# Optimization experiments

Measured on AMD Instinct MI355X. Metric: run time of the kernel, lower is better.

## Reference

```python
import jax, jax.numpy as jnp
import numpy as np

HIDDEN = 1024
NUM_HEADS = 16
HEAD_DIM = HIDDEN // NUM_HEADS
WINDOW = 512


def setup_inputs() -> dict:
    key = jax.random.key(0)
    ks = jax.random.split(key, 6)
    b, s = 2, 4096
    x = jax.random.normal(ks[0], (b, s, HIDDEN), dtype=jnp.float32)
    attention_mask = jnp.ones((b, s), dtype=jnp.int32)
    scale = 1.0 / np.sqrt(HIDDEN)
    Wq = jax.random.normal(ks[1], (HIDDEN, HIDDEN), dtype=jnp.float32) * scale
    Wk = jax.random.normal(ks[2], (HIDDEN, HIDDEN), dtype=jnp.float32) * scale
    Wv = jax.random.normal(ks[3], (HIDDEN, HIDDEN), dtype=jnp.float32) * scale
    Wo = jax.random.normal(ks[4], (HIDDEN, HIDDEN), dtype=jnp.float32) * scale
    return {"x": x, "attention_mask": attention_mask,
            "Wq": Wq, "Wk": Wk, "Wv": Wv, "Wo": Wo}


def reference(x, attention_mask, Wq, Wk, Wv, Wo):
    b, s, d = x.shape
    # nn.Linear computes x @ W.T
    q = (x @ Wq.T).reshape(b, s, NUM_HEADS, HEAD_DIM).transpose(0, 2, 1, 3)
    k = (x @ Wk.T).reshape(b, s, NUM_HEADS, HEAD_DIM).transpose(0, 2, 1, 3)
    v = (x @ Wv.T).reshape(b, s, NUM_HEADS, HEAD_DIM).transpose(0, 2, 1, 3)
    # [b,h,s,s] scores
    scores = jnp.einsum('bhqd,bhkd->bhqk', q, k) / np.sqrt(HEAD_DIM)
    # causal sliding-window mask: allow j <= i and j >= i - window + 1
    i = jnp.arange(s)[:, None]
    j = jnp.arange(s)[None, :]
    window_mask = (j <= i) & (j >= i - WINDOW + 1)  # [s,s]
    neg_inf = jnp.finfo(scores.dtype).min
    scores = jnp.where(window_mask[None, None], scores, neg_inf)
    pad = attention_mask.astype(bool)[:, None, None, :]  # [b,1,1,s]
    scores = jnp.where(pad, scores, neg_inf)
    probs = jax.nn.softmax(scores, axis=-1)
    out = jnp.einsum('bhqk,bhkd->bhqd', probs, v)
    out = out.transpose(0, 2, 1, 3).reshape(b, s, d)
    return out @ Wo.T
```

## Files before the change

### kernel.cpp

```cpp
#include <hip/hip_runtime.h>
#include <cstdint>
#include <cstddef>

#define HID 1024
#define SEQ 4096
#define NB  2
#define NH  16
#define HD  64
#define WIN 512
#define TOK (NB*SEQ)

typedef _Float16 f16x8 __attribute__((ext_vector_type(8)));
typedef _Float16 f16x4 __attribute__((ext_vector_type(4)));
typedef float    f32x4 __attribute__((ext_vector_type(4)));

__global__ __launch_bounds__(256)
void convert_kernel(const float* __restrict__ X, const float* __restrict__ w0,
                    const float* __restrict__ w1, const float* __restrict__ w2,
                    const float* __restrict__ w3,
                    _Float16* __restrict__ Xh, _Float16* __restrict__ Wh) {
  const int bi = blockIdx.x;
  const float* src; _Float16* dst; size_t off;
  if (bi < 4096) {
    src = X; dst = Xh; off = (size_t)bi * 2048;
  } else {
    const int wi = bi - 4096, z = wi >> 9;
    src = (z == 0) ? w0 : (z == 1) ? w1 : (z == 2) ? w2 : w3;
    dst = Wh + (size_t)z * HID * HID;
    off = (size_t)(wi & 511) * 2048;
  }
  const size_t i = off + (size_t)threadIdx.x * 8;
  f32x4 a = *(const f32x4*)(src + i);
  f32x4 b = *(const f32x4*)(src + i + 4);
  f16x8 o;
#pragma unroll
  for (int r = 0; r < 4; ++r) { o[r] = (_Float16)a[r]; o[r+4] = (_Float16)b[r]; }
  *(f16x8*)(dst + i) = o;
}

__device__ __forceinline__ void gload16(const void* g, void* lds) {
  __builtin_amdgcn_global_load_lds(
      (__attribute__((address_space(1))) void*)(void*)g,
      (__attribute__((address_space(3))) void*)lds, 16, 0, 0);
}

#define VMW_(n) asm volatile("s_waitcnt vmcnt(" #n ")" ::: "memory")
#define VMW(n) VMW_(n)

#define STG(GP, RP) {                                                         \
    gload16((GP) + (size_t)srow*HID + scol,     (RP) + ldo0);                 \
    gload16((GP) + (size_t)(srow+8)*HID + scol, (RP) + ldo1);                 \
  }

#define RDA(DST, HP) {                                                        \
    _Pragma("unroll")                                                         \
    for (int mm = 0; mm < 4; ++mm) {                                          \
      const int ar = (wr*16 + mm*32 + l15) * 64;                              \
      DST[mm][0] = *(const f16x8*)((HP) + ar + ((quad ^ swl) << 3));          \
      DST[mm][1] = *(const f16x8*)((HP) + ar + (((4 + quad) ^ swl) << 3));    \
    } }

#define RDB(DST, HP) {                                                        \
    _Pragma("unroll")                                                         \
    for (int nn = 0; nn < 2; ++nn) {                                          \
      const int br = (nn*64 + wc*16 + l15) * 64;                              \
      DST[nn][0] = *(const f16x8*)((HP) + br + ((quad ^ swl) << 3));          \
      DST[nn][1] = *(const f16x8*)((HP) + br + (((4 + quad) ^ swl) << 3));    \
    } }

#define CORE(QM, QN, AF, BV, VMN) {                                           \
    __builtin_amdgcn_s_barrier();                                             \
    __builtin_amdgcn_s_setprio(1);                                            \
    _Pragma("unroll")                                                         \
    for (int mm = 0; mm < 4; ++mm)                                            \
      _Pragma("unroll")                                                       \
      for (int nn = 0; nn < 2; ++nn) {                                        \
        acc[QM*4+mm][QN*2+nn] = __builtin_amdgcn_mfma_f32_16x16x32_f16(       \
            AF[mm][0], BV[nn][0], acc[QM*4+mm][QN*2+nn], 0, 0, 0);            \
        acc[QM*4+mm][QN*2+nn] = __builtin_amdgcn_mfma_f32_16x16x32_f16(       \
            AF[mm][1], BV[nn][1], acc[QM*4+mm][QN*2+nn], 0, 0, 0);            \
      }                                                                       \
    __builtin_amdgcn_s_setprio(0);                                            \
    VMW(VMN);                                                                 \
    __builtin_amdgcn_s_barrier();                                             \
    asm volatile("" ::: "memory");                                            \
  }

__global__ __launch_bounds__(512, 2)
void gemm_qkv8p_kernel(const _Float16* __restrict__ X,
                       const _Float16* __restrict__ Wh,
                       _Float16* __restrict__ Q,
                       _Float16* __restrict__ Kb,
                       _Float16* __restrict__ Vt) {
  __shared__ __align__(16) _Float16 sAb[2][2][128*64];
  __shared__ __align__(16) _Float16 sBb[2][2][128*64];

  const int bid = blockIdx.x;
  const int xcd = bid & 7, idx = bid >> 3;
  const int mt = xcd*4 + (idx & 3);
  const int nt = idx >> 2;
  const int M0  = mt * 256;
  const int N0g = nt * 256;
  const int z   = N0g >> 10;
  const int N0c = N0g & 1023;

  const _Float16* Arow = X  + (size_t)M0 * HID;
  const _Float16* Brow = Wh + (size_t)z * HID * HID + (size_t)N0c * HID;

  const int tid  = threadIdx.x;
  const int lane = tid & 63, wave = tid >> 6;
  const int wr = wave >> 2, wc = wave & 3;
  const int l15 = lane & 15, quad = lane >> 4;
  const int swl = l15 & 7;

  const int srow = wave*16 + (lane >> 3);
  const int scol = ((lane & 7) ^ (lane >> 3)) << 3;
  const int ldo0 = (wave*128 + lane) * 8;
  const int ldo1 = ldo0 + 64*8;

  f32x4 acc[8][4] = {};
  f16x8 af0[4][2], af1[4][2], bv0[2][2], bv1[2][2];

  STG(Brow,               sBb[0][0]);
  STG(Arow,               sAb[0][0]);
  STG(Arow + 128*HID,     sAb[0][1]);
  STG(Brow + 128*HID,     sBb[0][1]);
  STG(Brow + 64,          sBb[1][0]);
  STG(Arow + 64,          sAb[1][0]);
  VMW(8);
  __builtin_amdgcn_s_barrier();
  asm volatile("" ::: "memory");

  RDB(bv0, sBb[0][0]);

#pragma unroll 1
  for (int t = 0; t < 14; t += 2) {
    const int k1 = (t+1)*64, k2 = (t+2)*64, k3 = (t+3)*64;
    RDA(af0, sAb[0][0]);  STG(Arow + 128*HID + k1, sAb[1][1]);  CORE(0,0,af0,bv0,8);
    RDA(af1, sAb[0][1]);  STG(Brow + 128*HID + k1, sBb[1][1]);  CORE(1,0,af1,bv0,8);
    RDB(bv1, sBb[0][1]);  STG(Brow + k2,           sBb[0][0]);  CORE(1,1,af1,bv1,8);
    RDB(bv0, sBb[1][0]);  STG(Arow + k2,           sAb[0][0]);  CORE(0,1,af0,bv1,8);
    RDA(af0, sAb[1][0]);  STG(Arow + 128*HID + k2, sAb[0][1]);  CORE(0,0,af0,bv0,8);
    RDA(af1, sAb[1][1]);  STG(Brow + 128*HID + k2, sBb[0][1]);  CORE(1,0,af1,bv0,8);
    RDB(bv1, sBb[1][1]);  STG(Brow + k3,           sBb[1][0]);  CORE(1,1,af1,bv1,8);
    RDB(bv0, sBb[0][0]);  STG(Arow + k3,           sAb[1][0]);  CORE(0,1,af0,bv1,8);
  }
  {
    const int k1 = 15*64;
    RDA(af0, sAb[0][0]);  STG(Arow + 128*HID + k1, sAb[1][1]);  CORE(0,0,af0,bv0,8);
    RDA(af1, sAb[0][1]);  STG(Brow + 128*HID + k1, sBb[1][1]);  CORE(1,0,af1,bv0,8);
    RDB(bv1, sBb[0][1]);                                        CORE(1,1,af1,bv1,6);
    RDB(bv0, sBb[1][0]);                                        CORE(0,1,af0,bv1,4);
  }
  {
    RDA(af0, sAb[1][0]);                                        CORE(0,0,af0,bv0,2);
    RDA(af1, sAb[1][1]);                                        CORE(1,0,af1,bv0,0);
    RDB(bv1, sBb[1][1]);                                        CORE(1,1,af1,bv1,0);
                                                                CORE(0,1,af0,bv1,0);
  }

  if (z < 2) {
    _Float16* C = (z == 0) ? Q : Kb;
    const float scl = (z == 0) ? 0.18033688011f : 1.0f;
#pragma unroll
    for (int mf = 0; mf < 8; ++mf) {
      const int row = M0 + (mf >> 2)*128 + wr*16 + (mf & 3)*32 + quad*4;
#pragma unroll
      for (int nf = 0; nf < 4; ++nf) {
        const int col = N0c + (nf >> 1)*128 + (nf & 1)*64 + wc*16 + l15;
#pragma unroll
        for (int r = 0; r < 4; ++r)
          C[(size_t)(row + r)*HID + col] = (_Float16)(acc[mf][nf][r] * scl);
      }
    }
  } else {
#pragma unroll
    for (int mf = 0; mf < 8; ++mf) {
      const int row = M0 + (mf >> 2)*128 + wr*16 + (mf & 3)*32 + quad*4;
#pragma unroll
      for (int nf = 0; nf < 4; ++nf) {
        const int col = N0c + (nf >> 1)*128 + (nf & 1)*64 + wc*16 + l15;
        f16x4 v;
#pragma unroll
        for (int r = 0; r < 4; ++r) v[r] = (_Float16)acc[mf][nf][r];
        *(f16x4*)(Vt + (size_t)col*TOK + row) = v;
      }
    }
  }
}

__device__ __forceinline__ void gemm_mainloop(
    const _Float16* __restrict__ A, const _Float16* __restrict__ W,
    _Float16* sA, _Float16* sB, f32x4 (&acc)[4][4], int m0, int n0) {
  const int tid  = threadIdx.x;
  const int lane = tid & 63;
  const int wave = tid >> 6;
  const int wm = wave >> 1, wn = wave & 1;
  const int l15 = lane & 15, quad = lane >> 4;

  const int o0 = tid * 16;
  const int o1 = o0 + 4096;
  const _Float16* a0 = A + (size_t)(m0 + (o0 >> 6)) * HID + ((o0 & 63) >> 1);
  const _Float16* a1 = A + (size_t)(m0 + (o1 >> 6)) * HID + ((o1 & 63) >> 1);
  const _Float16* w0 = W + (size_t)(n0 + (o0 >> 6)) * HID + ((o0 & 63) >> 1);
  const _Float16* w1 = W + (size_t)(n0 + (o1 >> 6)) * HID + ((o1 & 63) >> 1);
  _Float16* la0 = sA + (o0 >> 1);
  _Float16* la1 = sA + (o1 >> 1);
  _Float16* lb0 = sB + (o0 >> 1);
  _Float16* lb1 = sB + (o1 >> 1);

  const int aoff = (wm*64 + l15)*32 + quad*8;
  const int boff = (wn*64 + l15)*32 + quad*8;

  for (int k0 = 0; k0 < HID; k0 += 64) {
    __syncthreads();
    gload16(a0 + k0,      la0);
    gload16(a1 + k0,      la1);
    gload16(a0 + k0 + 32, la0 + 4096);
    gload16(a1 + k0 + 32, la1 + 4096);
    gload16(w0 + k0,      lb0);
    gload16(w1 + k0,      lb1);
    gload16(w0 + k0 + 32, lb0 + 4096);
    gload16(w1 + k0 + 32, lb1 + 4096);
    __syncthreads();
#pragma unroll
    for (int s = 0; s < 2; ++s) {
      const int sb = s * 4096;
      f16x8 af[4], wf[4];
#pragma unroll
      for (int t = 0; t < 4; ++t) {
        af[t] = *(const f16x8*)(sA + sb + aoff + t*512);
        wf[t] = *(const f16x8*)(sB + sb + boff + t*512);
      }
#pragma unroll
      for (int i = 0; i < 4; ++i)
#pragma unroll
        for (int j = 0; j < 4; ++j)
          acc[i][j] = __builtin_amdgcn_mfma_f32_16x16x32_f16(af[i], wf[j], acc[i][j], 0, 0, 0);
    }
  }
}

__global__ __launch_bounds__(256, 3)
void gemm_o_kernel(const _Float16* __restrict__ A,
                   const _Float16* __restrict__ Wo,
                   float* __restrict__ C) {
  __shared__ __align__(16) _Float16 sA[128*64];
  __shared__ __align__(16) _Float16 sB[128*64];
  const int i  = blockIdx.x;
  const int g  = i & 7;
  const int j  = i >> 3;
  const int mi = j & 7;
  const int n0 = (j >> 3) * 128;
  const int m0 = (g*8 + mi) * 128;
  f32x4 acc[4][4] = {};
  gemm_mainloop(A, Wo, sA, sB, acc, m0, n0);

  const int tid  = threadIdx.x;
  const int lane = tid & 63;
  const int wave = tid >> 6;
  const int wm = wave >> 1, wn = wave & 1;
  const int l15 = lane & 15, quad = lane >> 4;
#pragma unroll
  for (int tm = 0; tm < 4; ++tm)
#pragma unroll
    for (int tn = 0; tn < 4; ++tn) {
      const int row = m0 + wm*64 + tm*16 + quad*4;
      const int col = n0 + wn*64 + tn*16 + l15;
#pragma unroll
      for (int r = 0; r < 4; ++r)
        C[(size_t)(row + r)*HID + col] = acc[tm][tn][r];
    }
}

__global__ __launch_bounds__(512, 4)
void attn_kernel(const _Float16* __restrict__ Q, const _Float16* __restrict__ Kb,
                 const _Float16* __restrict__ Vt, const int* __restrict__ AM,
                 _Float16* __restrict__ O) {
  __shared__ __align__(16) _Float16 sK[128*64];
  __shared__ __align__(16) _Float16 sV[64*128];
  __shared__ __align__(16) _Float16 sP[8*32*64];
  __shared__ int sOK;

  const int bi = blockIdx.x;
  const int g  = bi & 7;
  const int jj = bi >> 3;
  const int combo = g*4 + (jj >> 4);
  const int h = combo & 15, b = combo >> 4;
  const int qb = jj & 15;

  const int tid  = threadIdx.x;
  const int lane = tid & 63, wave = tid >> 6;
  const int l15 = lane & 15, quad = lane >> 4;

  const int q0 = qb * 256;
  const int qw = q0 + wave * 32;

  const int swz = l15 & 7;
  const int cA8 = ((quad ^ swz) << 3);
  const int cB8 = (((quad + 4) ^ swz) << 3);

  f16x8 qf[2][2];
#pragma unroll
  for (int ns = 0; ns < 2; ++ns) {
    const size_t qbse = (size_t)(b*SEQ + qw + ns*16 + l15)*HID + h*HD + quad*8;
    qf[ns][0] = *(const f16x8*)(Q + qbse);
    qf[ns][1] = *(const f16x8*)(Q + qbse + 32);
  }

  int stage_lo = (q0 - (WIN - 1));
  stage_lo = (stage_lo < 0) ? 0 : (stage_lo & ~127);
  const int nst = (q0 + 256 - stage_lo) >> 7;

  if (tid == 0) sOK = 1;
  __syncthreads();
  {
    int ok = 1;
    for (int j = stage_lo + tid; j < q0 + 256; j += 512) ok &= (AM[b*SEQ + j] != 0);
    if (!ok) sOK = 0;
  }
  __syncthreads();
  const bool allok = (sOK != 0);

  const int prow = tid >> 3;
  const int pc   = tid & 7;
  const int pco  = ((pc ^ (prow & 7)) << 3);
  f16x8 pk0, pk1, pv0, pv1;
  {
    const _Float16* kp = Kb + (size_t)(b*SEQ + stage_lo + prow)*HID + h*HD + pco;
    pk0 = *(const f16x8*)kp;
    pk1 = *(const f16x8*)(kp + (size_t)64*HID);
    const _Float16* vp = Vt + (size_t)(h*HD + prow)*TOK + b*SEQ + stage_lo + pco;
    pv0 = *(const f16x8*)vp;
    pv1 = *(const f16x8*)(vp + 64);
  }

  float l_run[2] = {0.0f, 0.0f};
  f32x4 o[4][2] = {};
  _Float16* myP = sP + wave * (32*64);

  for (int st = 0; st < nst; ++st) {
    const int j0st = stage_lo + st*128;
    __syncthreads();
    *(f16x8*)(sK + prow*64 + pc*8)        = pk0;
    *(f16x8*)(sK + (64 + prow)*64 + pc*8) = pk1;
    *(f16x8*)(sV + prow*128 + pc*8)       = pv0;
    *(f16x8*)(sV + prow*128 + 64 + pc*8)  = pv1;
    __syncthreads();
    if (st + 1 < nst) {
      const int jn = j0st + 128;
      const _Float16* kp = Kb + (size_t)(b*SEQ + jn + prow)*HID + h*HD + pco;
      pk0 = *(const f16x8*)kp;
      pk1 = *(const f16x8*)(kp + (size_t)64*HID);
      const _Float16* vp = Vt + (size_t)(h*HD + prow)*TOK + b*SEQ + jn + pco;
      pv0 = *(const f16x8*)vp;
      pv1 = *(const f16x8*)(vp + 64);
    }

#pragma unroll
    for (int s = 0; s < 2; ++s) {
      const int j0 = j0st + s*64;
      if (j0 > qw + 31 || j0 + 63 < qw - (WIN - 1)) continue;
      const bool interior = (j0 + 63 <= qw) && (j0 >= qw - (WIN - 32));

      f32x4 sc[4][2] = {};
#pragma unroll
      for (int t = 0; t < 4; ++t) {
        const f16x8 kf0 = *(const f16x8*)(sK + (s*64 + t*16 + l15)*64 + cA8);
        const f16x8 kf1 = *(const f16x8*)(sK + (s*64 + t*16 + l15)*64 + cB8);
        sc[t][0] = __builtin_amdgcn_mfma_f32_16x16x32_f16(kf0, qf[0][0], sc[t][0], 0, 0, 0);
        sc[t][0] = __builtin_amdgcn_mfma_f32_16x16x32_f16(kf1, qf[0][1], sc[t][0], 0, 0, 0);
        sc[t][1] = __builtin_amdgcn_mfma_f32_16x16x32_f16(kf0, qf[1][0], sc[t][1], 0, 0, 0);
        sc[t][1] = __builtin_amdgcn_mfma_f32_16x16x32_f16(kf1, qf[1][1], sc[t][1], 0, 0, 0);
      }

      if (!allok) {
#pragma unroll
        for (int t = 0; t < 4; ++t)
#pragma unroll
          for (int r = 0; r < 4; ++r) {
            const float ad = (AM[b*SEQ + j0 + t*16 + quad*4 + r] == 0) ? -2e30f : 0.0f;
            sc[t][0][r] += ad;
            sc[t][1][r] += ad;
          }
      }

#pragma unroll
      for (int ns = 0; ns < 2; ++ns) {
        if (!interior) {
          const int i = qw + ns*16 + l15;
#pragma unroll
          for (int t = 0; t < 4; ++t)
#pragma unroll
            for (int r = 0; r < 4; ++r) {
              const int j = j0 + t*16 + quad*4 + r;
              const bool valid = (unsigned)(i - j) < WIN;
              sc[t][ns][r] = valid ? sc[t][ns][r] : -1e30f;
            }
        }
        float sum = 0.0f;
#pragma unroll
        for (int t = 0; t < 4; ++t) {
          f16x4 pvv;
#pragma unroll
          for (int r = 0; r < 4; ++r) {
            const float p = __builtin_amdgcn_exp2f(sc[t][ns][r]);
            sum += p;
            pvv[r] = (_Float16)p;
          }
          const int paddr = (ns*16 + l15)*64 + (((2*t + (quad >> 1)) ^ swz) << 3) + (quad & 1)*4;
          *(f16x4*)(myP + paddr) = pvv;
        }
        sum += __shfl_xor(sum, 16, 64);
        sum += __shfl_xor(sum, 32, 64);
        l_run[ns] += sum;
      }

      const f16x8 pf00 = *(const f16x8*)(myP + l15*64 + cA8);
      const f16x8 pf01 = *(const f16x8*)(myP + l15*64 + cB8);
      const f16x8 pf10 = *(const f16x8*)(myP + (16 + l15)*64 + cA8);
      const f16x8 pf11 = *(const f16x8*)(myP + (16 + l15)*64 + cB8);
#pragma unroll
      for (int dt = 0; dt < 4; ++dt) {
        const f16x8 vf0 = *(const f16x8*)(sV + (dt*16 + l15)*128 + s*64 + cA8);
        const f16x8 vf1 = *(const f16x8*)(sV + (dt*16 + l15)*128 + s*64 + cB8);
        o[dt][0] = __builtin_amdgcn_mfma_f32_16x16x32_f16(vf0, pf00, o[dt][0], 0, 0, 0);
        o[dt][0] = __builtin_amdgcn_mfma_f32_16x16x32_f16(vf1, pf01, o[dt][0], 0, 0, 0);
        o[dt][1] = __builtin_amdgcn_mfma_f32_16x16x32_f16(vf0, pf10, o[dt][1], 0, 0, 0);
        o[dt][1] = __builtin_amdgcn_mfma_f32_16x16x32_f16(vf1, pf11, o[dt][1], 0, 0, 0);
      }
    }
  }

  const float inv[2] = {1.0f / fmaxf(l_run[0], 1e-30f), 1.0f / fmaxf(l_run[1], 1e-30f)};
#pragma unroll
  for (int ns = 0; ns < 2; ++ns) {
    const size_t ob = (size_t)(b*SEQ + qw + ns*16 + l15)*HID + h*HD + quad*4;
#pragma unroll
    for (int dt = 0; dt < 4; ++dt) {
      f16x4 v;
#pragma unroll
      for (int r = 0; r < 4; ++r) v[r] = (_Float16)(o[dt][ns][r] * inv[ns]);
      *(f16x4*)(O + ob + dt*16) = v;
    }
  }
}

extern "C" void kernel_launch(void* const* d_in, const int* in_sizes, int n_in,
                              void* d_out, int out_size, void* d_ws, size_t ws_size,
                              hipStream_t stream) {
  const float* X  = (const float*)d_in[0];
  const int*   AM = (const int*)d_in[1];
  const float* Wq = (const float*)d_in[2];
  const float* Wk = (const float*)d_in[3];
  const float* Wv = (const float*)d_in[4];
  const float* Wo = (const float*)d_in[5];
  float* out = (float*)d_out;

  _Float16* Xh = (_Float16*)d_ws;
  _Float16* Wh = Xh + (size_t)TOK*HID;
  _Float16* Qb = Wh + (size_t)4*HID*HID;
  _Float16* Kb = Qb + (size_t)TOK*HID;
  _Float16* Vt = Kb + (size_t)TOK*HID;
  _Float16* AO = Vt + (size_t)TOK*HID;

  convert_kernel<<<dim3(4096 + 4*512), dim3(256), 0, stream>>>(X, Wq, Wk, Wv, Wo, Xh, Wh);
  gemm_qkv8p_kernel<<<dim3(384), dim3(512), 0, stream>>>(Xh, Wh, Qb, Kb, Vt);
  attn_kernel<<<dim3(512), dim3(512), 0, stream>>>(Qb, Kb, Vt, AM, AO);
  gemm_o_kernel<<<dim3(512), dim3(256), 0, stream>>>(AO, Wh + (size_t)3*HID*HID, out);
}
```

Baseline: 240.8 us.

## Reschedule QKV GEMM main loop with one barrier per MFMA phase

Rewrites the software pipeline of the QKV projection GEMM. Each phase now uses a single barrier instead of two, prefetches deeper (four stages in flight at the prologue), and splits A-fragment LDS reads into halves interleaved with MFMA phases in a new order. The aim is to cut barrier stalls and hide LDS and global latency behind matrix math. In exchange the waitcnt and barrier ordering is more fragile, and any hazard in the schedule could corrupt data or add stalls.

Result: slower. 291.6 us (+21.1%).

```diff
diff --git a/kernel.cpp b/kernel.cpp
--- a/kernel.cpp
+++ b/kernel.cpp
@@ -44,17 +44,16 @@
       (__attribute__((address_space(3))) void*)lds, 16, 0, 0);
 }
 
-#define VMW_(n) asm volatile("s_waitcnt vmcnt(" #n ")" ::: "memory")
-#define VMW(n) VMW_(n)
+#define VMW(n) asm volatile("s_waitcnt vmcnt(" #n ")" ::: "memory")
 
 #define STG(GP, RP) {                                                         \
     gload16((GP) + (size_t)srow*HID + scol,     (RP) + ldo0);                 \
     gload16((GP) + (size_t)(srow+8)*HID + scol, (RP) + ldo1);                 \
   }
 
-#define RDA(DST, HP) {                                                        \
+#define RDA2(DST, HP, MM0) {                                                  \
     _Pragma("unroll")                                                         \
-    for (int mm = 0; mm < 4; ++mm) {                                          \
+    for (int mm = MM0; mm < MM0+2; ++mm) {                                    \
       const int ar = (wr*16 + mm*32 + l15) * 64;                              \
       DST[mm][0] = *(const f16x8*)((HP) + ar + ((quad ^ swl) << 3));          \
       DST[mm][1] = *(const f16x8*)((HP) + ar + (((4 + quad) ^ swl) << 3));    \
@@ -68,8 +67,7 @@
       DST[nn][1] = *(const f16x8*)((HP) + br + (((4 + quad) ^ swl) << 3));    \
     } }
 
-#define CORE(QM, QN, AF, BV, VMN) {                                           \
-    __builtin_amdgcn_s_barrier();                                             \
+#define MMA(QM, QN, AF, BV) {                                                 \
     __builtin_amdgcn_s_setprio(1);                                            \
     _Pragma("unroll")                                                         \
     for (int mm = 0; mm < 4; ++mm)                                            \
@@ -81,10 +79,9 @@
             AF[mm][1], BV[nn][1], acc[QM*4+mm][QN*2+nn], 0, 0, 0);            \
       }                                                                       \
     __builtin_amdgcn_s_setprio(0);                                            \
-    VMW(VMN);                                                                 \
-    __builtin_amdgcn_s_barrier();                                             \
-    asm volatile("" ::: "memory");                                            \
-  }
+  }
+
+#define BAR() __builtin_amdgcn_s_barrier()
 
 __global__ __launch_bounds__(512, 2)
 void gemm_qkv8p_kernel(const _Float16* __restrict__ X,
@@ -121,43 +118,65 @@
   f32x4 acc[8][4] = {};
   f16x8 af0[4][2], af1[4][2], bv0[2][2], bv1[2][2];
 
-  STG(Brow,               sBb[0][0]);
-  STG(Arow,               sAb[0][0]);
-  STG(Arow + 128*HID,     sAb[0][1]);
-  STG(Brow + 128*HID,     sBb[0][1]);
-  STG(Brow + 64,          sBb[1][0]);
-  STG(Arow + 64,          sAb[1][0]);
+  STG(Arow,                sAb[0][0]);
+  STG(Brow,                sBb[0][0]);
+  STG(Brow + 128*HID,      sBb[0][1]);
+  STG(Arow + 128*HID,      sAb[0][1]);
+  STG(Arow + 64,           sAb[1][0]);
+  STG(Brow + 128*HID + 64, sBb[1][1]);
+  STG(Brow + 64,           sBb[1][0]);
+  STG(Arow + 128*HID + 64, sAb[1][1]);
+  VMW(12);
+  BAR();
+  RDA2(af0, sAb[0][0], 0);
+  RDA2(af0, sAb[0][0], 2);
+  RDB(bv0, sBb[0][0]);
   VMW(8);
-  __builtin_amdgcn_s_barrier();
-  asm volatile("" ::: "memory");
-
-  RDB(bv0, sBb[0][0]);
 
 #pragma unroll 1
   for (int t = 0; t < 14; t += 2) {
-    const int k1 = (t+1)*64, k2 = (t+2)*64, k3 = (t+3)*64;
-    RDA(af0, sAb[0][0]);  STG(Arow + 128*HID + k1, sAb[1][1]);  CORE(0,0,af0,bv0,8);
-    RDA(af1, sAb[0][1]);  STG(Brow + 128*HID + k1, sBb[1][1]);  CORE(1,0,af1,bv0,8);
-    RDB(bv1, sBb[0][1]);  STG(Brow + k2,           sBb[0][0]);  CORE(1,1,af1,bv1,8);
-    RDB(bv0, sBb[1][0]);  STG(Arow + k2,           sAb[0][0]);  CORE(0,1,af0,bv1,8);
-    RDA(af0, sAb[1][0]);  STG(Arow + 128*HID + k2, sAb[0][1]);  CORE(0,0,af0,bv0,8);
-    RDA(af1, sAb[1][1]);  STG(Brow + 128*HID + k2, sBb[0][1]);  CORE(1,0,af1,bv0,8);
-    RDB(bv1, sBb[1][1]);  STG(Brow + k3,           sBb[1][0]);  CORE(1,1,af1,bv1,8);
-    RDB(bv0, sBb[0][0]);  STG(Arow + k3,           sAb[1][0]);  CORE(0,1,af0,bv1,8);
-  }
-  {
-    const int k1 = 15*64;
-    RDA(af0, sAb[0][0]);  STG(Arow + 128*HID + k1, sAb[1][1]);  CORE(0,0,af0,bv0,8);
-    RDA(af1, sAb[0][1]);  STG(Brow + 128*HID + k1, sBb[1][1]);  CORE(1,0,af1,bv0,8);
-    RDB(bv1, sBb[0][1]);                                        CORE(1,1,af1,bv1,6);
-    RDB(bv0, sBb[1][0]);                                        CORE(0,1,af0,bv1,4);
-  }
-  {
-    RDA(af0, sAb[1][0]);                                        CORE(0,0,af0,bv0,2);
-    RDA(af1, sAb[1][1]);                                        CORE(1,0,af1,bv0,0);
-    RDB(bv1, sBb[1][1]);                                        CORE(1,1,af1,bv1,0);
-                                                                CORE(0,1,af0,bv1,0);
-  }
+    const int kt2 = (t+2)*64;
+    const int kt3 = (t+3)*64;
+    BAR();  RDB(bv1, sBb[0][1]);  RDA2(af1, sAb[0][1], 0);
+            MMA(0,0, af0, bv0);  VMW(8);
+    BAR();  STG(Arow + kt2,            sAb[0][0]);
+            RDA2(af1, sAb[0][1], 2);
+            MMA(0,1, af0, bv1);  VMW(8);
+    BAR();  STG(Brow + 128*HID + kt2,  sBb[0][1]);
+            STG(Brow + kt2,            sBb[0][0]);
+            RDA2(af0, sAb[1][0], 0);
+            MMA(1,1, af1, bv1);  VMW(8);
+    BAR();  STG(Arow + 128*HID + kt2,  sAb[0][1]);
+            RDA2(af0, sAb[1][0], 2);  RDB(bv1, sBb[1][1]);
+            MMA(1,0, af1, bv0);  VMW(8);
+    BAR();  RDB(bv0, sBb[1][0]);  RDA2(af1, sAb[1][1], 0);
+            MMA(0,1, af0, bv1);  VMW(8);
+    BAR();  STG(Arow + kt3,            sAb[1][0]);
+            RDA2(af1, sAb[1][1], 2);
+            MMA(0,0, af0, bv0);  VMW(8);
+    BAR();  STG(Brow + 128*HID + kt3,  sBb[1][1]);
+            STG(Brow + kt3,            sBb[1][0]);
+            RDA2(af0, sAb[0][0], 0);
+            MMA(1,0, af1, bv0);  VMW(8);
+    BAR();  STG(Arow + 128*HID + kt3,  sAb[1][1]);
+            RDA2(af0, sAb[0][0], 2);  RDB(bv0, sBb[0][0]);
+            MMA(1,1, af1, bv1);  VMW(8);
+  }
+
+  BAR();  RDB(bv1, sBb[0][1]);  RDA2(af1, sAb[0][1], 0);
+          MMA(0,0, af0, bv0);  VMW(8);
+  BAR();  RDA2(af1, sAb[0][1], 2);
+          MMA(0,1, af0, bv1);  VMW(6);
+  BAR();  RDA2(af0, sAb[1][0], 0);
+          MMA(1,1, af1, bv1);  VMW(2);
+  BAR();  RDA2(af0, sAb[1][0], 2);  RDB(bv1, sBb[1][1]);
+          MMA(1,0, af1, bv0);  VMW(0);
+  BAR();  RDB(bv0, sBb[1][0]);  RDA2(af1, sAb[1][1], 0);
+          MMA(0,1, af0, bv1);
+  BAR();  RDA2(af1, sAb[1][1], 2);
+          MMA(0,0, af0, bv0);
+          MMA(1,0, af1, bv0);
+          MMA(1,1, af1, bv1);
 
   if (z < 2) {
     _Float16* C = (z == 0) ? Q : Kb;
```
